# Kernel optimization log

Hardware: AMD Instinct MI355X
Metric: run time of the kernel (lower is better)

## Reference

```python
import jax, jax.numpy as jnp
import numpy as np

B, S, D = 8, 2048, 512
Q, K = 8, 1024


def setup_inputs() -> dict:
    key = jax.random.key(0)
    k1, k2 = jax.random.split(key)
    x = jax.random.normal(k1, (B, S, D), dtype=jnp.float32)
    codebooks = jax.random.normal(k2, (Q, K, D), dtype=jnp.float32) * 0.02
    return {"x": x, "codebooks": codebooks}


def reference(x, codebooks):
    """Residual VQ forward (eval mode): per level cdist + argmin + gather.

    Returns (quantized, indices, commitment_loss, perplexity) matching the
    torch module's output dict.
    """
    b, s, d = x.shape
    q_levels, k_codes, _ = codebooks.shape
    xf = x.reshape(-1, d)              # (N, D), N = b*s
    n_tok = xf.shape[0]

    def step(carry, codebook):
        residual, qsum = carry
        # squared euclidean distances: ||r||^2 - 2 r.C^T + ||c||^2  -> (N, K)
        dists = (
            jnp.sum(residual * residual, axis=-1, keepdims=True)
            - 2.0 * (residual @ codebook.T)
            + jnp.sum(codebook * codebook, axis=-1)[None, :]
        )
        idx = jnp.argmin(dists, axis=-1)          # (N,)
        quant = codebook[idx]                     # (N, D) gather
        commit = jnp.mean((residual - jax.lax.stop_gradient(quant)) ** 2)
        counts = jnp.zeros((k_codes,), x.dtype).at[idx].add(1.0)
        avg_probs = counts / n_tok
        perp = jnp.exp(-jnp.sum(avg_probs * jnp.log(avg_probs + 1e-10)))
        return (residual - quant, qsum + quant), (idx, commit, perp)

    (_, quantized_sum), (all_idx, commits, perps) = jax.lax.scan(
        step, (xf, jnp.zeros_like(xf)), codebooks
    )

    commitment_weight = 0.25
    commitment_loss = jnp.sum(commits) * commitment_weight
    perplexity = jnp.mean(perps)
    indices = jnp.transpose(all_idx).reshape(b, s, q_levels)  # (B, S, Q)
    # straight-through estimator
    quantized = x + jax.lax.stop_gradient(quantized_sum.reshape(b, s, d) - x)
    return quantized, indices, commitment_loss, perplexity
```

## Files before the change

### kernel.cpp

```cpp
#include <hip/hip_runtime.h>
#include <math.h>

#define NTOK 16384
#define DIM 512
#define QLV 8
#define KCODE 1024
#define BM 64
#define DC 8
#define NCH (DIM / DC)
#define TAU 1e-3f

#define NCK 16
#define CHUNKB 131072
#define CBSPLIT_FLOAT_OFF 65536
#define RCAP 16

typedef __attribute__((ext_vector_type(4))) float f32x4;
typedef __attribute__((ext_vector_type(8))) short bf16x8;

__global__ __launch_bounds__(256) void zero_ws(float* ws) {
  int i = blockIdx.x * 256 + threadIdx.x;
  for (int k = i; k < QLV * KCODE + 2 * QLV; k += gridDim.x * 256) ws[k] = 0.f;
}

__device__ __forceinline__ float np_blk128_sq(const float* __restrict__ x) {
#pragma clang fp contract(off)
  float L[16];
#pragma unroll
  for (int j = 0; j < 16; ++j) {
    const float a0 = x[j] * x[j];
    const float a1 = x[16 + j] * x[16 + j];
    const float a2 = x[32 + j] * x[32 + j];
    const float a3 = x[48 + j] * x[48 + j];
    const float a4 = x[64 + j] * x[64 + j];
    const float a5 = x[80 + j] * x[80 + j];
    const float a6 = x[96 + j] * x[96 + j];
    const float a7 = x[112 + j] * x[112 + j];
    L[j] = ((a0 + a1) + (a2 + a3)) + ((a4 + a5) + (a6 + a7));
  }
  float T3[8];
#pragma unroll
  for (int i = 0; i < 8; ++i) T3[i] = L[i] + L[i + 8];
  float T6[4];
#pragma unroll
  for (int j = 0; j < 4; ++j) T6[j] = T3[j] + T3[j + 4];
  return (T6[0] + T6[2]) + (T6[1] + T6[3]);
}

__device__ __forceinline__ float np_sum512_sq(const float* __restrict__ x) {
#pragma clang fp contract(off)
  const float p0 = np_blk128_sq(x);
  const float p1 = np_blk128_sq(x + 128);
  const float p2 = np_blk128_sq(x + 256);
  const float p3 = np_blk128_sq(x + 384);
  const float s01 = p0 + p1;
  const float s23 = p2 + p3;
  return s01 + s23;
}

__device__ __forceinline__ float np_dist(float A, const float* __restrict__ r,
                                         const float* __restrict__ c, float cn) {
#pragma clang fp contract(off)
  float b1 = 0.f;
#pragma unroll 8
  for (int d = 0; d < 384; ++d) b1 = __builtin_fmaf(r[d], c[d], b1);
  float b2 = 0.f;
#pragma unroll 8
  for (int d = 384; d < 512; ++d) b2 = __builtin_fmaf(r[d], c[d], b2);
  const float B = b1 + b2;
  const float t1 = 2.0f * B;
  const float t2 = A - t1;
  return t2 + cn;
}

__global__ __launch_bounds__(256) void cnorm_np_kernel(const float* __restrict__ cb,
                                                       float* __restrict__ cn) {
  const int row = blockIdx.x * 256 + threadIdx.x;
  cn[row] = np_sum512_sq(cb + (size_t)row * DIM);
}

__device__ __forceinline__ bool lt2(float a, int ia, float b, int ib) {
  return a < b || (a == b && ia < ib);
}

__device__ __forceinline__ unsigned short bf16_rtne(float x) {
  unsigned u = __builtin_bit_cast(unsigned, x);
  u += 0x7FFFu + ((u >> 16) & 1u);
  return (unsigned short)(u >> 16);
}
__device__ __forceinline__ float bf16_tof(unsigned short h) {
  unsigned u = (unsigned)h << 16;
  return __builtin_bit_cast(float, u);
}
__device__ __forceinline__ void split2(float x, unsigned short& h, unsigned short& l) {
  h = bf16_rtne(x);
  l = bf16_rtne(x - bf16_tof(h));
}

__device__ __forceinline__ void gload16(const void* g, void* l) {
  __builtin_amdgcn_global_load_lds(
      (const __attribute__((address_space(1))) unsigned int*)g,
      (__attribute__((address_space(3))) unsigned int*)l, 16, 0, 0);
}

__global__ __launch_bounds__(256) void split_cb_kernel(const float* __restrict__ cb,
                                                       unsigned short* __restrict__ dst) {
  const int f = blockIdx.x * 256 + threadIdx.x;
  const int d4 = f & 127;
  const int c = (f >> 7) & 1023;
  const int q = f >> 17;
  const float4 v = *(const float4*)(cb + (size_t)f * 4);
  const int d0 = d4 * 4;
  const int dc = d0 >> 5;
  const int e = d0 & 31;
  const int kb = e >> 3;
  const int e7 = e & 7;
  const int half = c >> 9, cl = c & 511;
  const int slot = kb ^ ((cl >> 1) & 3);
  const size_t base = (size_t)(q * NCK + dc) * CHUNKB + (size_t)half * 65536;
  const size_t off = base + (size_t)cl * 64 + (size_t)slot * 16 + (size_t)e7 * 2;
  unsigned short h0, l0, h1, l1, h2, l2, h3, l3;
  split2(v.x, h0, l0);
  split2(v.y, h1, l1);
  split2(v.z, h2, l2);
  split2(v.w, h3, l3);
  uint2 hv, lv;
  hv.x = (unsigned)h0 | ((unsigned)h1 << 16);
  hv.y = (unsigned)h2 | ((unsigned)h3 << 16);
  lv.x = (unsigned)l0 | ((unsigned)l1 << 16);
  lv.y = (unsigned)l2 | ((unsigned)l3 << 16);
  char* db = (char*)dst;
  *(uint2*)(db + off) = hv;
  *(uint2*)(db + off + 32768) = lv;
}

template <bool FIRST, bool LAST>
__global__ __launch_bounds__(512, 2) void level_mfma(
    const float* __restrict__ x, float* __restrict__ resid,
    const float* __restrict__ cb, const unsigned short* __restrict__ cbsplit,
    const float* __restrict__ cnorm, float* __restrict__ out_idx,
    float* __restrict__ counts, float* __restrict__ commit, int* __restrict__ rcnt,
    int* __restrict__ rlist, int* __restrict__ cand_cnt, int* __restrict__ cand,
    int have_cand, int qlev) {
  __shared__ __align__(16) unsigned char Bs[131072];
  __shared__ __align__(16) unsigned char As[16384];
  __shared__ __align__(16) float foldb[64][8][4];
  __shared__ int chosen[64];
  __shared__ float tieV1[64];
  __shared__ int ccnt[64];

  const int tid = threadIdx.x;
  const int lane = tid & 63;
  const int w = tid >> 6;
  const int col = lane & 15;
  const int kb = lane >> 4;
  const int blk = blockIdx.x;
  const float* rin = FIRST ? x : resid;
  const char* csp = (const char*)cbsplit;
  const size_t wl = (size_t)w * 8192 + (size_t)lane * 16;

  const int arow = tid >> 3;
  const int ae0 = (tid & 7) * 4;
  const int akb = ae0 >> 3;
  const int aslot = akb ^ ((arow >> 1) & 3);
  const size_t abyte = (size_t)arow * 64 + (size_t)aslot * 16 + (size_t)(ae0 & 7) * 2;
  const float* aglob = rin + (size_t)(blk * BM + arow) * DIM + ae0;

  f32x4 acc[2][4][4];
#pragma unroll
  for (int h = 0; h < 2; ++h)
#pragma unroll
    for (int j = 0; j < 4; ++j)
#pragma unroll
      for (int tf = 0; tf < 4; ++tf) acc[h][j][tf] = (f32x4){0.f, 0.f, 0.f, 0.f};

  {
    const float4 pA = *(const float4*)aglob;
    unsigned short h0, l0, h1, l1, h2, l2, h3, l3;
    split2(pA.x, h0, l0);
    split2(pA.y, h1, l1);
    split2(pA.z, h2, l2);
    split2(pA.w, h3, l3);
    uint2 hv, lv;
    hv.x = (unsigned)h0 | ((unsigned)h1 << 16);
    hv.y = (unsigned)h2 | ((unsigned)h3 << 16);
    lv.x = (unsigned)l0 | ((unsigned)l1 << 16);
    lv.y = (unsigned)l2 | ((unsigned)l3 << 16);
    *(uint2*)&As[abyte] = hv;
    *(uint2*)&As[4096 + abyte] = lv;
  }
  {
    const char* s = csp + wl;
    unsigned char* d = &Bs[(size_t)w * 8192];
#pragma unroll
    for (int i = 0; i < 8; ++i) gload16(s + i * 1024, d + i * 1024);
  }
  {
    const char* s = csp + 65536 + wl;
    unsigned char* d = &Bs[65536 + (size_t)w * 8192];
#pragma unroll
    for (int i = 0; i < 8; ++i) gload16(s + i * 1024, d + i * 1024);
  }
  asm volatile("s_waitcnt lgkmcnt(0)" ::: "memory");

  for (int dc = 0; dc < NCK; ++dc) {
    const int dn = (dc + 1) & (NCK - 1);
    const int abuf = dc & 1;
    const char* srcN = csp + (size_t)dn * CHUNKB;

    asm volatile("s_waitcnt vmcnt(8)" ::: "memory");
    asm volatile("s_barrier" ::: "memory");
    const float4 pAn = *(const float4*)(aglob + dn * 32);

    bf16x8 ah[4], al[4];
#pragma unroll
    for (int tf = 0; tf < 4; ++tf) {
      const int row = tf * 16 + col;
      const size_t slot16 = (size_t)((kb ^ ((row >> 1) & 3)) * 16);
      const size_t ab = (size_t)abuf * 8192 + (size_t)row * 64 + slot16;
      ah[tf] = *(const bf16x8*)&As[ab];
      al[tf] = *(const bf16x8*)&As[ab + 4096];
    }
    bf16x8 b0h[4], b0l[4];
#pragma unroll
    for (int j = 0; j < 4; ++j) {
      const int cl = (w + 8 * j) * 16 + col;
      const size_t bb = (size_t)cl * 64 + (size_t)((kb ^ ((cl >> 1) & 3)) * 16);
      b0h[j] = *(const bf16x8*)&Bs[bb];
      b0l[j] = *(const bf16x8*)&Bs[32768 + bb];
    }
    asm volatile("s_waitcnt lgkmcnt(0)" ::: "memory");
    __builtin_amdgcn_sched_barrier(0);
    __builtin_amdgcn_s_setprio(1);
#pragma unroll
    for (int j = 0; j < 4; ++j)
#pragma unroll
      for (int tf = 0; tf < 4; ++tf) {
        acc[0][j][tf] = __builtin_amdgcn_mfma_f32_16x16x32_bf16(ah[tf], b0h[j], acc[0][j][tf], 0, 0, 0);
        acc[0][j][tf] = __builtin_amdgcn_mfma_f32_16x16x32_bf16(al[tf], b0h[j], acc[0][j][tf], 0, 0, 0);
        acc[0][j][tf] = __builtin_amdgcn_mfma_f32_16x16x32_bf16(ah[tf], b0l[j], acc[0][j][tf], 0, 0, 0);
      }
    __builtin_amdgcn_s_setprio(0);
    asm volatile("s_barrier" ::: "memory");
    {
      const char* s = srcN + wl;
      unsigned char* d = &Bs[(size_t)w * 8192];
#pragma unroll
      for (int i = 0; i < 8; ++i) gload16(s + i * 1024, d + i * 1024);
    }

    asm volatile("s_waitcnt vmcnt(9)" ::: "memory");
    asm volatile("s_barrier" ::: "memory");
    {
      unsigned short h0, l0, h1, l1, h2, l2, h3, l3;
      split2(pAn.x, h0, l0);
      split2(pAn.y, h1, l1);
      split2(pAn.z, h2, l2);
      split2(pAn.w, h3, l3);
      uint2 hv, lv;
      hv.x = (unsigned)h0 | ((unsigned)h1 << 16);
      hv.y = (unsigned)h2 | ((unsigned)h3 << 16);
      lv.x = (unsigned)l0 | ((unsigned)l1 << 16);
      lv.y = (unsigned)l2 | ((unsigned)l3 << 16);
      const size_t ab0 = (size_t)(abuf ^ 1) * 8192 + abyte;
      *(uint2*)&As[ab0] = hv;
      *(uint2*)&As[ab0 + 4096] = lv;
    }
    bf16x8 b1h[4], b1l[4];
#pragma unroll
    for (int j = 0; j < 4; ++j) {
      const int cl = (w + 8 * j) * 16 + col;
      const size_t bb = (size_t)cl * 64 + (size_t)((kb ^ ((cl >> 1) & 3)) * 16);
      b1h[j] = *(const bf16x8*)&Bs[65536 + bb];
      b1l[j] = *(const bf16x8*)&Bs[65536 + 32768 + bb];
    }
    asm volatile("s_waitcnt lgkmcnt(0)" ::: "memory");
    __builtin_amdgcn_sched_barrier(0);
    __builtin_amdgcn_s_setprio(1);
#pragma unroll
    for (int j = 0; j < 4; ++j)
#pragma unroll
      for (int tf = 0; tf < 4; ++tf) {
        acc[1][j][tf] = __builtin_amdgcn_mfma_f32_16x16x32_bf16(ah[tf], b1h[j], acc[1][j][tf], 0, 0, 0);
        acc[1][j][tf] = __builtin_amdgcn_mfma_f32_16x16x32_bf16(al[tf], b1h[j], acc[1][j][tf], 0, 0, 0);
        acc[1][j][tf] = __builtin_amdgcn_mfma_f32_16x16x32_bf16(ah[tf], b1l[j], acc[1][j][tf], 0, 0, 0);
      }
    __builtin_amdgcn_s_setprio(0);
    asm volatile("s_barrier" ::: "memory");
    {
      const char* s = srcN + 65536 + wl;
      unsigned char* d = &Bs[65536 + (size_t)w * 8192];
#pragma unroll
      for (int i = 0; i < 8; ++i) gload16(s + i * 1024, d + i * 1024);
    }
  }
  __syncthreads();

  float cnv[2][4];
#pragma unroll
  for (int h = 0; h < 2; ++h)
#pragma unroll
    for (int j = 0; j < 4; ++j) cnv[h][j] = cnorm[(h * 32 + w + 8 * j) * 16 + col];

#pragma unroll
  for (int tf = 0; tf < 4; ++tf) {
#pragma unroll
    for (int r = 0; r < 4; ++r) {
      float b1 = 3.4e38f, b2 = 3.4e38f;
      int x1 = KCODE, x2 = KCODE;
#pragma unroll
      for (int h = 0; h < 2; ++h)
#pragma unroll
        for (int j = 0; j < 4; ++j) {
          const int c = (h * 32 + w + 8 * j) * 16 + col;
          const float dist = fmaf(-2.f, acc[h][j][tf][r], cnv[h][j]);
          if (lt2(dist, c, b1, x1)) {
            b2 = b1; x2 = x1; b1 = dist; x1 = c;
          } else if (lt2(dist, c, b2, x2)) {
            b2 = dist; x2 = c;
          }
        }
#pragma unroll
      for (int off = 1; off < 16; off <<= 1) {
        const float w1 = __shfl_xor(b1, off);
        const int j1 = __shfl_xor(x1, off);
        const float w2 = __shfl_xor(b2, off);
        const int j2 = __shfl_xor(x2, off);
        if (lt2(w1, j1, b1, x1)) {
          if (lt2(b1, x1, w2, j2)) { b2 = b1; x2 = x1; }
          else { b2 = w2; x2 = j2; }
          b1 = w1; x1 = j1;
        } else if (lt2(w1, j1, b2, x2)) {
          b2 = w1; x2 = j1;
        }
      }
      if (col == 0) {
        const int t = tf * 16 + (lane >> 4) * 4 + r;
        float4 fv;
        fv.x = b1; fv.y = __int_as_float(x1); fv.z = b2; fv.w = __int_as_float(x2);
        *(float4*)&foldb[t][w][0] = fv;
      }
    }
  }
  __syncthreads();

  if (tid < 64) {
    float V1 = 3.4e38f, V2 = 3.4e38f;
    int I1 = KCODE, I2 = KCODE;
#pragma unroll
    for (int ww = 0; ww < 8; ++ww) {
      const float4 e = *(const float4*)&foldb[tid][ww][0];
      const float a1 = e.x, a2 = e.z;
      const int a1i = __float_as_int(e.y), a2i = __float_as_int(e.w);
      if (lt2(a1, a1i, V1, I1)) {
        if (lt2(V1, I1, a2, a2i)) { V2 = V1; I2 = I1; }
        else { V2 = a2; I2 = a2i; }
        V1 = a1; I1 = a1i;
      } else if (lt2(a1, a1i, V2, I2)) {
        V2 = a1; I2 = a1i;
      }
    }
    ccnt[tid] = 0;
    tieV1[tid] = V1;
    if (V2 - V1 < TAU) {
      const int pos = atomicAdd(rcnt, 1);
      rlist[pos] = blk * BM + tid;
      chosen[tid] = -1;
    } else {
      chosen[tid] = I1;
      out_idx[(size_t)(blk * BM + tid) * QLV + qlev] = (float)I1;
      atomicAdd(&counts[I1], 1.0f);
    }
  }
  __syncthreads();

  if (have_cand) {
#pragma unroll
    for (int tf = 0; tf < 4; ++tf)
#pragma unroll
      for (int r = 0; r < 4; ++r) {
        const int t = tf * 16 + (lane >> 4) * 4 + r;
        if (chosen[t] != -1) continue;
        const float thr = tieV1[t] + TAU;
#pragma unroll
        for (int h = 0; h < 2; ++h)
#pragma unroll
          for (int j = 0; j < 4; ++j) {
            const float dist = fmaf(-2.f, acc[h][j][tf][r], cnv[h][j]);
            if (dist < thr) {
              const int c = (h * 32 + w + 8 * j) * 16 + col;
              const int pos = atomicAdd(&ccnt[t], 1);
              if (pos < RCAP) cand[(size_t)(blk * BM + t) * RCAP + pos] = c;
            }
          }
      }
    __syncthreads();
    if (tid < 64 && chosen[tid] == -1) cand_cnt[blk * BM + tid] = ccnt[tid];
  }

  {
    const int tb = tid >> 3, part = tid & 7;
    const size_t tok = (size_t)(blk * BM + tb);
    const int idx = chosen[tb];
    float sq = 0.f;
    if (idx >= 0) {
      const float4* cp = (const float4*)(cb + (size_t)idx * DIM);
      const float4* rp = (const float4*)(rin + tok * DIM);
      const float4* xp = (const float4*)(x + tok * DIM);
      float4* op = (float4*)(resid + tok * DIM);
#pragma unroll 4
      for (int kk = 0; kk < 16; ++kk) {
        const int d4 = part + kk * 8;
        const float4 r = rp[d4], c4 = cp[d4];
        float4 rn;
        rn.x = r.x - c4.x; rn.y = r.y - c4.y; rn.z = r.z - c4.z; rn.w = r.w - c4.w;
        sq += rn.x * rn.x + rn.y * rn.y + rn.z * rn.z + rn.w * rn.w;
        if (LAST) {
          const float4 xv = xp[d4];
          float4 qv;
          qv.x = xv.x - rn.x; qv.y = xv.y - rn.y; qv.z = xv.z - rn.z; qv.w = xv.w - rn.w;
          op[d4] = qv;
        } else {
          op[d4] = rn;
        }
      }
    }
#pragma unroll
    for (int off = 32; off; off >>= 1) sq += __shfl_down(sq, off);
    if (lane == 0) atomicAdd(commit, sq);
  }
}

template <bool FIRST, bool LAST>
__global__ __launch_bounds__(512, 2) void level_kernel(
    const float* __restrict__ x, float* __restrict__ resid,
    const float* __restrict__ cb, const float* __restrict__ cnorm,
    float* __restrict__ out_idx, float* __restrict__ counts,
    float* __restrict__ commit, int* __restrict__ rcnt,
    int* __restrict__ rlist, int qlev) {
  __shared__ float Rs[DC][BM + 4];
  __shared__ float Cs[DC][KCODE + 4];
  __shared__ int chosen[BM];

  const int tid = threadIdx.x;
  const int lane = tid & 63;
  const int ty = tid >> 6;
  const int tx = lane;
  const int blk = blockIdx.x;
  const float* rin = FIRST ? x : resid;

  float acc[8][16];
#pragma unroll
  for (int j = 0; j < 8; ++j)
#pragma unroll
    for (int g = 0; g < 16; ++g) acc[j][g] = 0.f;

  float4 pc[4];
  float4 pr;
  {
#pragma unroll
    for (int u = 0; u < 4; ++u) {
      const int f4 = tid + u * 512;
      const int code = f4 >> 1, d4 = f4 & 1;
      pc[u] = *(const float4*)(cb + (size_t)code * DIM + d4 * 4);
    }
    if (tid < 128) {
      const int tok = tid >> 1, d4 = tid & 1;
      pr = *(const float4*)(rin + (size_t)(blk * BM + tok) * DIM + d4 * 4);
    }
  }

  for (int dc = 0; dc < NCH; ++dc) {
    __syncthreads();
#pragma unroll
    for (int u = 0; u < 4; ++u) {
      const int f4 = tid + u * 512;
      const int code = f4 >> 1, d4 = f4 & 1;
      Cs[d4 * 4 + 0][code] = pc[u].x;
      Cs[d4 * 4 + 1][code] = pc[u].y;
      Cs[d4 * 4 + 2][code] = pc[u].z;
      Cs[d4 * 4 + 3][code] = pc[u].w;
    }
    if (tid < 128) {
      const int tok = tid >> 1, d4 = tid & 1;
      Rs[d4 * 4 + 0][tok] = pr.x;
      Rs[d4 * 4 + 1][tok] = pr.y;
      Rs[d4 * 4 + 2][tok] = pr.z;
      Rs[d4 * 4 + 3][tok] = pr.w;
    }
    if (dc + 1 < NCH) {
      const int doff = (dc + 1) * DC;
#pragma unroll
      for (int u = 0; u < 4; ++u) {
        const int f4 = tid + u * 512;
        const int code = f4 >> 1, d4 = f4 & 1;
        pc[u] = *(const float4*)(cb + (size_t)code * DIM + doff + d4 * 4);
      }
      if (tid < 128) {
        const int tok = tid >> 1, d4 = tid & 1;
        pr = *(const float4*)(rin + (size_t)(blk * BM + tok) * DIM + doff + d4 * 4);
      }
    }
    __syncthreads();
#pragma unroll
    for (int d = 0; d < DC; ++d) {
      const float4 ra = *(const float4*)&Rs[d][ty * 8];
      const float4 rb = *(const float4*)&Rs[d][ty * 8 + 4];
#pragma unroll
      for (int q = 0; q < 4; ++q) {
        const float4 cv = *(const float4*)&Cs[d][q * 256 + tx * 4];
        const float c0 = cv.x, c1 = cv.y, c2 = cv.z, c3 = cv.w;
        acc[0][q * 4 + 0] = fmaf(ra.x, c0, acc[0][q * 4 + 0]);
        acc[0][q * 4 + 1] = fmaf(ra.x, c1, acc[0][q * 4 + 1]);
        acc[0][q * 4 + 2] = fmaf(ra.x, c2, acc[0][q * 4 + 2]);
        acc[0][q * 4 + 3] = fmaf(ra.x, c3, acc[0][q * 4 + 3]);
        acc[1][q * 4 + 0] = fmaf(ra.y, c0, acc[1][q * 4 + 0]);
        acc[1][q * 4 + 1] = fmaf(ra.y, c1, acc[1][q * 4 + 1]);
        acc[1][q * 4 + 2] = fmaf(ra.y, c2, acc[1][q * 4 + 2]);
        acc[1][q * 4 + 3] = fmaf(ra.y, c3, acc[1][q * 4 + 3]);
        acc[2][q * 4 + 0] = fmaf(ra.z, c0, acc[2][q * 4 + 0]);
        acc[2][q * 4 + 1] = fmaf(ra.z, c1, acc[2][q * 4 + 1]);
        acc[2][q * 4 + 2] = fmaf(ra.z, c2, acc[2][q * 4 + 2]);
        acc[2][q * 4 + 3] = fmaf(ra.z, c3, acc[2][q * 4 + 3]);
        acc[3][q * 4 + 0] = fmaf(ra.w, c0, acc[3][q * 4 + 0]);
        acc[3][q * 4 + 1] = fmaf(ra.w, c1, acc[3][q * 4 + 1]);
        acc[3][q * 4 + 2] = fmaf(ra.w, c2, acc[3][q * 4 + 2]);
        acc[3][q * 4 + 3] = fmaf(ra.w, c3, acc[3][q * 4 + 3]);
        acc[4][q * 4 + 0] = fmaf(rb.x, c0, acc[4][q * 4 + 0]);
        acc[4][q * 4 + 1] = fmaf(rb.x, c1, acc[4][q * 4 + 1]);
        acc[4][q * 4 + 2] = fmaf(rb.x, c2, acc[4][q * 4 + 2]);
        acc[4][q * 4 + 3] = fmaf(rb.x, c3, acc[4][q * 4 + 3]);
        acc[5][q * 4 + 0] = fmaf(rb.y, c0, acc[5][q * 4 + 0]);
        acc[5][q * 4 + 1] = fmaf(rb.y, c1, acc[5][q * 4 + 1]);
        acc[5][q * 4 + 2] = fmaf(rb.y, c2, acc[5][q * 4 + 2]);
        acc[5][q * 4 + 3] = fmaf(rb.y, c3, acc[5][q * 4 + 3]);
        acc[6][q * 4 + 0] = fmaf(rb.z, c0, acc[6][q * 4 + 0]);
        acc[6][q * 4 + 1] = fmaf(rb.z, c1, acc[6][q * 4 + 1]);
        acc[6][q * 4 + 2] = fmaf(rb.z, c2, acc[6][q * 4 + 2]);
        acc[6][q * 4 + 3] = fmaf(rb.z, c3, acc[6][q * 4 + 3]);
        acc[7][q * 4 + 0] = fmaf(rb.w, c0, acc[7][q * 4 + 0]);
        acc[7][q * 4 + 1] = fmaf(rb.w, c1, acc[7][q * 4 + 1]);
        acc[7][q * 4 + 2] = fmaf(rb.w, c2, acc[7][q * 4 + 2]);
        acc[7][q * 4 + 3] = fmaf(rb.w, c3, acc[7][q * 4 + 3]);
      }
    }
  }

  float v1[8], v2[8];
  int i1[8], i2[8];
#pragma unroll
  for (int j = 0; j < 8; ++j) { v1[j] = v2[j] = 3.4e38f; i1[j] = i2[j] = KCODE; }
#pragma unroll
  for (int g = 0; g < 16; ++g) {
    const int c = (g >> 2) * 256 + tx * 4 + (g & 3);
    const float cn = cnorm[c];
#pragma unroll
    for (int j = 0; j < 8; ++j) {
      const float dist = fmaf(-2.f, acc[j][g], cn);
      if (lt2(dist, c, v1[j], i1[j])) {
        v2[j] = v1[j]; i2[j] = i1[j]; v1[j] = dist; i1[j] = c;
      } else if (lt2(dist, c, v2[j], i2[j])) {
        v2[j] = dist; i2[j] = c;
      }
    }
  }
#pragma unroll
  for (int off = 1; off < 64; off <<= 1) {
#pragma unroll
    for (int j = 0; j < 8; ++j) {
      const float w1 = __shfl_xor(v1[j], off);
      const int j1 = __shfl_xor(i1[j], off);
      const float w2 = __shfl_xor(v2[j], off);
      const int j2 = __shfl_xor(i2[j], off);
      if (lt2(w1, j1, v1[j], i1[j])) {
        if (lt2(v1[j], i1[j], w2, j2)) { v2[j] = v1[j]; i2[j] = i1[j]; }
        else { v2[j] = w2; i2[j] = j2; }
        v1[j] = w1; i1[j] = j1;
      } else {
        if (lt2(w1, j1, v2[j], i2[j])) { v2[j] = w1; i2[j] = j1; }
      }
    }
  }
  if (lane < 8) {
    const int tb = ty * 8 + lane;
    const float V1 = v1[lane], V2 = v2[lane];
    const int I1 = i1[lane];
    if (V2 - V1 < TAU) {
      const int pos = atomicAdd(rcnt, 1);
      rlist[pos] = blk * BM + tb;
      chosen[tb] = -1;
    } else {
      chosen[tb] = I1;
      out_idx[(size_t)(blk * BM + tb) * QLV + qlev] = (float)I1;
      atomicAdd(&counts[I1], 1.0f);
    }
  }
  __syncthreads();
  {
    const int tb = tid >> 3, part = tid & 7;
    const size_t tok = (size_t)(blk * BM + tb);
    const int idx = chosen[tb];
    float sq = 0.f;
    if (idx >= 0) {
      const float4* cp = (const float4*)(cb + (size_t)idx * DIM);
      const float4* rp = (const float4*)(rin + tok * DIM);
      const float4* xp = (const float4*)(x + tok * DIM);
      float4* op = (float4*)(resid + tok * DIM);
#pragma unroll 4
      for (int kk = 0; kk < 16; ++kk) {
        const int d4 = part + kk * 8;
        const float4 r = rp[d4], c4 = cp[d4];
        float4 rn;
        rn.x = r.x - c4.x; rn.y = r.y - c4.y; rn.z = r.z - c4.z; rn.w = r.w - c4.w;
        sq += rn.x * rn.x + rn.y * rn.y + rn.z * rn.z + rn.w * rn.w;
        if (LAST) {
          const float4 xv = xp[d4];
          float4 qv;
          qv.x = xv.x - rn.x; qv.y = xv.y - rn.y; qv.z = xv.z - rn.z; qv.w = xv.w - rn.w;
          op[d4] = qv;
        } else {
          op[d4] = rn;
        }
      }
    }
#pragma unroll
    for (int off = 32; off; off >>= 1) sq += __shfl_down(sq, off);
    if (lane == 0) atomicAdd(commit, sq);
  }
}

template <bool LAST>
__global__ __launch_bounds__(256) void rescue_np(
    const float* __restrict__ x, const float* __restrict__ rin,
    float* __restrict__ resid, const float* __restrict__ cbq,
    const float* __restrict__ cnq, float* __restrict__ out_idx,
    float* __restrict__ counts, float* __restrict__ commit,
    const int* __restrict__ rcnt, const int* __restrict__ rlist,
    const int* __restrict__ cand_cnt, const int* __restrict__ cand,
    int have_cand, int qlev) {
  __shared__ float rsh[DIM];
  __shared__ __align__(16) float crows[RCAP][DIM];
  __shared__ float sA;
  __shared__ float wv[4];
  __shared__ int wi[4];
  __shared__ int bestk_s;
  const int tid = threadIdx.x;
  const int n = rcnt[0];
  for (int it = blockIdx.x; it < n; it += gridDim.x) {
    const int t = rlist[it];
    rsh[tid] = rin[(size_t)t * DIM + tid];
    rsh[256 + tid] = rin[(size_t)t * DIM + 256 + tid];
    __syncthreads();
    if (tid == 0) sA = np_sum512_sq(rsh);
    __syncthreads();
    const float A = sA;
    float bv = 3.4e38f;
    int bi = KCODE;
    const int m = have_cand ? cand_cnt[t] : (RCAP + 1);
    if (m <= RCAP) {
      for (int c = 0; c < m; ++c) {
        const int k = cand[(size_t)t * RCAP + c];
        crows[c][tid] = cbq[(size_t)k * DIM + tid];
        crows[c][256 + tid] = cbq[(size_t)k * DIM + 256 + tid];
      }
      __syncthreads();
      for (int c = tid; c < m; c += 256) {
        const int k = cand[(size_t)t * RCAP + c];
        const float d = np_dist(A, rsh, &crows[c][0], cnq[k]);
        if (d < bv || (d == bv && k < bi)) { bv = d; bi = k; }
      }
    } else {
      for (int kk = 0; kk < 4; ++kk) {
        const int k = tid * 4 + kk;
        const float d = np_dist(A, rsh, cbq + (size_t)k * DIM, cnq[k]);
        if (d < bv) { bv = d; bi = k; }
      }
    }
#pragma unroll
    for (int off = 32; off; off >>= 1) {
      const float ov = __shfl_down(bv, off);
      const int oi = __shfl_down(bi, off);
      if (ov < bv || (ov == bv && oi < bi)) { bv = ov; bi = oi; }
    }
    if ((tid & 63) == 0) { wv[tid >> 6] = bv; wi[tid >> 6] = bi; }
    __syncthreads();
    if (tid == 0) {
      float V = wv[0]; int I = wi[0];
#pragma unroll
      for (int w = 1; w < 4; ++w)
        if (wv[w] < V || (wv[w] == V && wi[w] < I)) { V = wv[w]; I = wi[w]; }
      bestk_s = I;
      out_idx[(size_t)t * QLV + qlev] = (float)I;
      atomicAdd(&counts[I], 1.0f);
    }
    __syncthreads();
    const float* crow = cbq + (size_t)bestk_s * DIM;
    float sq;
    {
      const int d0 = tid, d1 = tid + 256;
      const float rn0 = rsh[d0] - crow[d0];
      const float rn1 = rsh[d1] - crow[d1];
      sq = rn0 * rn0 + rn1 * rn1;
      if (LAST) {
        resid[(size_t)t * DIM + d0] = x[(size_t)t * DIM + d0] - rn0;
        resid[(size_t)t * DIM + d1] = x[(size_t)t * DIM + d1] - rn1;
      } else {
        resid[(size_t)t * DIM + d0] = rn0;
        resid[(size_t)t * DIM + d1] = rn1;
      }
    }
#pragma unroll
    for (int off = 32; off; off >>= 1) sq += __shfl_down(sq, off);
    if ((tid & 63) == 0) wv[tid >> 6] = sq;
    __syncthreads();
    if (tid == 0)
      atomicAdd(commit, wv[0] + wv[1] + wv[2] + wv[3]);
    __syncthreads();
  }
}

__global__ __launch_bounds__(256) void finalize_scalars(const float* __restrict__ counts,
                                                        const float* __restrict__ commit,
                                                        float* __restrict__ out2) {
  const int tid = threadIdx.x;
  __shared__ float sh[4];
  __shared__ float perp_acc;
  if (tid == 0) perp_acc = 0.f;
  __syncthreads();
  for (int q = 0; q < QLV; ++q) {
    float h = 0.f;
    for (int k = tid; k < KCODE; k += 256) {
      const float p = counts[q * KCODE + k] * (1.0f / (float)NTOK);
      h += p * logf(p + 1e-10f);
    }
#pragma unroll
    for (int off = 32; off; off >>= 1) h += __shfl_down(h, off);
    if ((tid & 63) == 0) sh[tid >> 6] = h;
    __syncthreads();
    if (tid == 0) {
      const float H = sh[0] + sh[1] + sh[2] + sh[3];
      perp_acc += expf(-H);
    }
    __syncthreads();
  }
  if (tid == 0) {
    float closs = 0.f;
    for (int q = 0; q < QLV; ++q) closs += commit[q];
    out2[0] = closs * (0.25f / ((float)NTOK * (float)DIM));
    out2[1] = perp_acc * (1.0f / (float)QLV);
  }
}

extern "C" void kernel_launch(void* const* d_in, const int* in_sizes, int n_in,
                              void* d_out, int out_size, void* d_ws, size_t ws_size,
                              hipStream_t stream) {
  const float* x = (const float*)d_in[0];
  const float* cb = (const float*)d_in[1];
  float* out = (float*)d_out;
  float* ws = (float*)d_ws;

  float* resid = out;
  float* oidx = out + (size_t)NTOK * DIM;
  float* scal = oidx + (size_t)NTOK * QLV;
  float* counts = ws;
  float* commit = ws + QLV * KCODE;
  int* rcnt = (int*)(ws + QLV * KCODE + QLV);
  float* cnorm = ws + QLV * KCODE + 512;
  int* rlist = (int*)(ws + QLV * KCODE + 512 + QLV * KCODE);
  unsigned short* cbsplit = (unsigned short*)(ws + CBSPLIT_FLOAT_OFF);

  const size_t csplit_floats = (size_t)QLV * NCK * CHUNKB / 4;
  int* cand_cnt = (int*)(ws + CBSPLIT_FLOAT_OFF + csplit_floats);
  int* cand = cand_cnt + NTOK;
  const size_t need_mfma = ((size_t)CBSPLIT_FLOAT_OFF + csplit_floats) * 4;
  const size_t need_cand = need_mfma + (size_t)NTOK * (RCAP + 1) * 4;
  const bool use_mfma = ws_size >= need_mfma;
  const int have_cand = (use_mfma && ws_size >= need_cand) ? 1 : 0;

  hipLaunchKernelGGL(zero_ws, dim3(32), dim3(256), 0, stream, ws);
  hipLaunchKernelGGL(cnorm_np_kernel, dim3((QLV * KCODE) / 256), dim3(256), 0, stream,
                     cb, cnorm);
  if (use_mfma)
    hipLaunchKernelGGL(split_cb_kernel, dim3((QLV * KCODE * DIM / 4) / 256), dim3(256), 0,
                       stream, cb, cbsplit);

  for (int q = 0; q < QLV; ++q) {
    const float* cbq = cb + (size_t)q * KCODE * DIM;
    const float* cnq = cnorm + q * KCODE;
    float* ctq = counts + q * KCODE;
    float* cmq = commit + q;
    int* rcq = rcnt + q;
    const float* rin = (q == 0) ? x : resid;
    if (use_mfma) {
      const unsigned short* csq = cbsplit + (size_t)q * (NCK * CHUNKB / 2);
      if (q == 0)
        hipLaunchKernelGGL((level_mfma<true, false>), dim3(NTOK / BM), dim3(512), 0, stream,
                           x, resid, cbq, csq, cnq, oidx, ctq, cmq, rcq, rlist,
                           cand_cnt, cand, have_cand, q);
      else if (q == QLV - 1)
        hipLaunchKernelGGL((level_mfma<false, true>), dim3(NTOK / BM), dim3(512), 0, stream,
                           x, resid, cbq, csq, cnq, oidx, ctq, cmq, rcq, rlist,
                           cand_cnt, cand, have_cand, q);
      else
        hipLaunchKernelGGL((level_mfma<false, false>), dim3(NTOK / BM), dim3(512), 0, stream,
                           x, resid, cbq, csq, cnq, oidx, ctq, cmq, rcq, rlist,
                           cand_cnt, cand, have_cand, q);
    } else {
      if (q == 0)
        hipLaunchKernelGGL((level_kernel<true, false>), dim3(NTOK / BM), dim3(512), 0, stream,
                           x, resid, cbq, cnq, oidx, ctq, cmq, rcq, rlist, q);
      else if (q == QLV - 1)
        hipLaunchKernelGGL((level_kernel<false, true>), dim3(NTOK / BM), dim3(512), 0, stream,
                           x, resid, cbq, cnq, oidx, ctq, cmq, rcq, rlist, q);
      else
        hipLaunchKernelGGL((level_kernel<false, false>), dim3(NTOK / BM), dim3(512), 0, stream,
                           x, resid, cbq, cnq, oidx, ctq, cmq, rcq, rlist, q);
    }
    if (q == QLV - 1)
      hipLaunchKernelGGL((rescue_np<true>), dim3(256), dim3(256), 0, stream,
                         x, rin, resid, cbq, cnq, oidx, ctq, cmq, rcq, rlist,
                         cand_cnt, cand, have_cand, q);
    else
      hipLaunchKernelGGL((rescue_np<false>), dim3(256), dim3(256), 0, stream,
                         x, rin, resid, cbq, cnq, oidx, ctq, cmq, rcq, rlist,
                         cand_cnt, cand, have_cand, q);
  }
  hipLaunchKernelGGL(finalize_scalars, dim3(1), dim3(256), 0, stream, counts, commit, scal);
}
```

Measured before the change: 1.166 ms.

## Replace block-shared B double buffer with per-wave ring buffer streaming

```diff
diff --git a/kernel.cpp b/kernel.cpp
--- a/kernel.cpp
+++ b/kernel.cpp
@@ -134,6 +134,8 @@
   *(uint2*)(db + off + 32768) = lv;
 }
 
+#define VMW(N) asm volatile("s_waitcnt vmcnt(" #N ")" ::: "memory")
+
 template <bool FIRST, bool LAST>
 __global__ __launch_bounds__(512, 2) void level_mfma(
     const float* __restrict__ x, float* __restrict__ resid,
@@ -142,7 +144,7 @@
     float* __restrict__ counts, float* __restrict__ commit, int* __restrict__ rcnt,
     int* __restrict__ rlist, int* __restrict__ cand_cnt, int* __restrict__ cand,
     int have_cand, int qlev) {
-  __shared__ __align__(16) unsigned char Bs[131072];
+  __shared__ __align__(16) unsigned char Bring[8][8][2048];
   __shared__ __align__(16) unsigned char As[16384];
   __shared__ __align__(16) float foldb[64][8][4];
   __shared__ int chosen[64];
@@ -157,7 +159,21 @@
   const int blk = blockIdx.x;
   const float* rin = FIRST ? x : resid;
   const char* csp = (const char*)cbsplit;
-  const size_t wl = (size_t)w * 8192 + (size_t)lane * 16;
+  unsigned char* bringw = &Bring[w][0][0];
+  const int bcol = col * 64 + ((kb ^ ((col >> 1) & 3)) << 4);
+
+  size_t srcoff[8];
+#pragma unroll
+  for (int jp = 0; jp < 8; ++jp) {
+    const int cf = w + 8 * jp;
+    srcoff[jp] = (size_t)(cf >> 5) * 65536 + (size_t)(cf & 31) * 1024 + (size_t)lane * 16;
+  }
+  int rdA[4];
+#pragma unroll
+  for (int tf = 0; tf < 4; ++tf) {
+    const int row = tf * 16 + col;
+    rdA[tf] = row * 64 + ((kb ^ ((row >> 1) & 3)) << 4);
+  }
 
   const int arow = tid >> 3;
   const int ae0 = (tid & 7) * 4;
@@ -166,141 +182,107 @@
   const size_t abyte = (size_t)arow * 64 + (size_t)aslot * 16 + (size_t)(ae0 & 7) * 2;
   const float* aglob = rin + (size_t)(blk * BM + arow) * DIM + ae0;
 
-  f32x4 acc[2][4][4];
-#pragma unroll
-  for (int h = 0; h < 2; ++h)
-#pragma unroll
-    for (int j = 0; j < 4; ++j)
-#pragma unroll
-      for (int tf = 0; tf < 4; ++tf) acc[h][j][tf] = (f32x4){0.f, 0.f, 0.f, 0.f};
+  f32x4 acc[8][4];
+#pragma unroll
+  for (int j = 0; j < 8; ++j)
+#pragma unroll
+    for (int tf = 0; tf < 4; ++tf) acc[j][tf] = (f32x4){0.f, 0.f, 0.f, 0.f};
+
+#define LM_ISSUE(PDC, JP)                                          \
+  {                                                                \
+    const char* s_ = csp + (size_t)(PDC)*CHUNKB + srcoff[JP];      \
+    unsigned char* d_ = bringw + (JP)*2048;                        \
+    gload16(s_, d_);                                               \
+    gload16(s_ + 32768, d_ + 1024);                                \
+  }
+
+#define LM_COMPUTE(JJ)                                                                   \
+  {                                                                                      \
+    const unsigned char* sb_ = bringw + (JJ)*2048 + bcol;                                \
+    const bf16x8 bh_ = *(const bf16x8*)sb_;                                              \
+    const bf16x8 bl_ = *(const bf16x8*)(sb_ + 1024);                                     \
+    __builtin_amdgcn_s_setprio(1);                                                       \
+    _Pragma("unroll") for (int tf = 0; tf < 4; ++tf) {                                   \
+      acc[JJ][tf] = __builtin_amdgcn_mfma_f32_16x16x32_bf16(ah[tf], bh_, acc[JJ][tf], 0, 0, 0); \
+      acc[JJ][tf] = __builtin_amdgcn_mfma_f32_16x16x32_bf16(al[tf], bh_, acc[JJ][tf], 0, 0, 0); \
+      acc[JJ][tf] = __builtin_amdgcn_mfma_f32_16x16x32_bf16(ah[tf], bl_, acc[JJ][tf], 0, 0, 0); \
+    }                                                                                    \
+    __builtin_amdgcn_s_setprio(0);                                                       \
+  }
+
+#define LM_ASPLIT(BUF)                                             \
+  {                                                                \
+    unsigned short h0, l0, h1, l1, h2, l2, h3, l3;                 \
+    split2(pAn.x, h0, l0);                                         \
+    split2(pAn.y, h1, l1);                                         \
+    split2(pAn.z, h2, l2);                                         \
+    split2(pAn.w, h3, l3);                                         \
+    uint2 hv, lv;                                                  \
+    hv.x = (unsigned)h0 | ((unsigned)h1 << 16);                    \
+    hv.y = (unsigned)h2 | ((unsigned)h3 << 16);                    \
+    lv.x = (unsigned)l0 | ((unsigned)l1 << 16);                    \
+    lv.y = (unsigned)l2 | ((unsigned)l3 << 16);                    \
+    const size_t ab0_ = (size_t)(BUF)*8192 + abyte;                \
+    *(uint2*)&As[ab0_] = hv;                                       \
+    *(uint2*)&As[4096 + ab0_] = lv;                                \
+  }
 
   {
-    const float4 pA = *(const float4*)aglob;
-    unsigned short h0, l0, h1, l1, h2, l2, h3, l3;
-    split2(pA.x, h0, l0);
-    split2(pA.y, h1, l1);
-    split2(pA.z, h2, l2);
-    split2(pA.w, h3, l3);
-    uint2 hv, lv;
-    hv.x = (unsigned)h0 | ((unsigned)h1 << 16);
-    hv.y = (unsigned)h2 | ((unsigned)h3 << 16);
-    lv.x = (unsigned)l0 | ((unsigned)l1 << 16);
-    lv.y = (unsigned)l2 | ((unsigned)l3 << 16);
-    *(uint2*)&As[abyte] = hv;
-    *(uint2*)&As[4096 + abyte] = lv;
-  }
-  {
-    const char* s = csp + wl;
-    unsigned char* d = &Bs[(size_t)w * 8192];
-#pragma unroll
-    for (int i = 0; i < 8; ++i) gload16(s + i * 1024, d + i * 1024);
-  }
-  {
-    const char* s = csp + 65536 + wl;
-    unsigned char* d = &Bs[65536 + (size_t)w * 8192];
-#pragma unroll
-    for (int i = 0; i < 8; ++i) gload16(s + i * 1024, d + i * 1024);
+    const float4 pAn = *(const float4*)aglob;
+    LM_ISSUE(0, 0); LM_ISSUE(0, 1); LM_ISSUE(0, 2);
+    LM_ISSUE(0, 3); LM_ISSUE(0, 4); LM_ISSUE(0, 5);
+    LM_ASPLIT(0);
   }
   asm volatile("s_waitcnt lgkmcnt(0)" ::: "memory");
-
-  for (int dc = 0; dc < NCK; ++dc) {
-    const int dn = (dc + 1) & (NCK - 1);
+  __builtin_amdgcn_s_barrier();
+
+  for (int dc = 0; dc < NCK - 1; ++dc) {
     const int abuf = dc & 1;
-    const char* srcN = csp + (size_t)dn * CHUNKB;
-
-    asm volatile("s_waitcnt vmcnt(8)" ::: "memory");
-    asm volatile("s_barrier" ::: "memory");
-    const float4 pAn = *(const float4*)(aglob + dn * 32);
-
     bf16x8 ah[4], al[4];
 #pragma unroll
     for (int tf = 0; tf < 4; ++tf) {
-      const int row = tf * 16 + col;
-      const size_t slot16 = (size_t)((kb ^ ((row >> 1) & 3)) * 16);
-      const size_t ab = (size_t)abuf * 8192 + (size_t)row * 64 + slot16;
+      const size_t ab = (size_t)abuf * 8192 + (size_t)rdA[tf];
       ah[tf] = *(const bf16x8*)&As[ab];
       al[tf] = *(const bf16x8*)&As[ab + 4096];
     }
-    bf16x8 b0h[4], b0l[4];
-#pragma unroll
-    for (int j = 0; j < 4; ++j) {
-      const int cl = (w + 8 * j) * 16 + col;
-      const size_t bb = (size_t)cl * 64 + (size_t)((kb ^ ((cl >> 1) & 3)) * 16);
-      b0h[j] = *(const bf16x8*)&Bs[bb];
-      b0l[j] = *(const bf16x8*)&Bs[32768 + bb];
-    }
+    float4 pAn;
+    VMW(10); LM_ISSUE(dc, 6);
+    pAn = *(const float4*)(aglob + (dc + 1) * 32);
+    LM_COMPUTE(0);
+    VMW(11); LM_ISSUE(dc, 7);     LM_COMPUTE(1);
+    VMW(11); LM_ISSUE(dc + 1, 0); LM_COMPUTE(2);
+    VMW(11); LM_ISSUE(dc + 1, 1); LM_COMPUTE(3);
+    VMW(11); LM_ISSUE(dc + 1, 2); LM_COMPUTE(4);
+    VMW(11); LM_ISSUE(dc + 1, 3); LM_COMPUTE(5);
+    LM_ASPLIT(abuf ^ 1);
+    VMW(11); LM_ISSUE(dc + 1, 4); LM_COMPUTE(6);
+    VMW(10); LM_ISSUE(dc + 1, 5); LM_COMPUTE(7);
     asm volatile("s_waitcnt lgkmcnt(0)" ::: "memory");
-    __builtin_amdgcn_sched_barrier(0);
-    __builtin_amdgcn_s_setprio(1);
-#pragma unroll
-    for (int j = 0; j < 4; ++j)
-#pragma unroll
-      for (int tf = 0; tf < 4; ++tf) {
-        acc[0][j][tf] = __builtin_amdgcn_mfma_f32_16x16x32_bf16(ah[tf], b0h[j], acc[0][j][tf], 0, 0, 0);
-        acc[0][j][tf] = __builtin_amdgcn_mfma_f32_16x16x32_bf16(al[tf], b0h[j], acc[0][j][tf], 0, 0, 0);
-        acc[0][j][tf] = __builtin_amdgcn_mfma_f32_16x16x32_bf16(ah[tf], b0l[j], acc[0][j][tf], 0, 0, 0);
-      }
-    __builtin_amdgcn_s_setprio(0);
-    asm volatile("s_barrier" ::: "memory");
-    {
-      const char* s = srcN + wl;
-      unsigned char* d = &Bs[(size_t)w * 8192];
-#pragma unroll
-      for (int i = 0; i < 8; ++i) gload16(s + i * 1024, d + i * 1024);
-    }
-
-    asm volatile("s_waitcnt vmcnt(9)" ::: "memory");
-    asm volatile("s_barrier" ::: "memory");
-    {
-      unsigned short h0, l0, h1, l1, h2, l2, h3, l3;
-      split2(pAn.x, h0, l0);
-      split2(pAn.y, h1, l1);
-      split2(pAn.z, h2, l2);
-      split2(pAn.w, h3, l3);
-      uint2 hv, lv;
-      hv.x = (unsigned)h0 | ((unsigned)h1 << 16);
-      hv.y = (unsigned)h2 | ((unsigned)h3 << 16);
-      lv.x = (unsigned)l0 | ((unsigned)l1 << 16);
-      lv.y = (unsigned)l2 | ((unsigned)l3 << 16);
-      const size_t ab0 = (size_t)(abuf ^ 1) * 8192 + abyte;
-      *(uint2*)&As[ab0] = hv;
-      *(uint2*)&As[ab0 + 4096] = lv;
-    }
-    bf16x8 b1h[4], b1l[4];
-#pragma unroll
-    for (int j = 0; j < 4; ++j) {
-      const int cl = (w + 8 * j) * 16 + col;
-      const size_t bb = (size_t)cl * 64 + (size_t)((kb ^ ((cl >> 1) & 3)) * 16);
-      b1h[j] = *(const bf16x8*)&Bs[65536 + bb];
-      b1l[j] = *(const bf16x8*)&Bs[65536 + 32768 + bb];
-    }
-    asm volatile("s_waitcnt lgkmcnt(0)" ::: "memory");
-    __builtin_amdgcn_sched_barrier(0);
-    __builtin_amdgcn_s_setprio(1);
-#pragma unroll
-    for (int j = 0; j < 4; ++j)
-#pragma unroll
-      for (int tf = 0; tf < 4; ++tf) {
-        acc[1][j][tf] = __builtin_amdgcn_mfma_f32_16x16x32_bf16(ah[tf], b1h[j], acc[1][j][tf], 0, 0, 0);
-        acc[1][j][tf] = __builtin_amdgcn_mfma_f32_16x16x32_bf16(al[tf], b1h[j], acc[1][j][tf], 0, 0, 0);
-        acc[1][j][tf] = __builtin_amdgcn_mfma_f32_16x16x32_bf16(ah[tf], b1l[j], acc[1][j][tf], 0, 0, 0);
-      }
-    __builtin_amdgcn_s_setprio(0);
-    asm volatile("s_barrier" ::: "memory");
-    {
-      const char* s = srcN + 65536 + wl;
-      unsigned char* d = &Bs[65536 + (size_t)w * 8192];
-#pragma unroll
-      for (int i = 0; i < 8; ++i) gload16(s + i * 1024, d + i * 1024);
-    }
+    __builtin_amdgcn_s_barrier();
+  }
+
+  {
+    bf16x8 ah[4], al[4];
+#pragma unroll
+    for (int tf = 0; tf < 4; ++tf) {
+      const size_t ab = (size_t)8192 + (size_t)rdA[tf];
+      ah[tf] = *(const bf16x8*)&As[ab];
+      al[tf] = *(const bf16x8*)&As[ab + 4096];
+    }
+    VMW(10); LM_ISSUE(15, 6); LM_COMPUTE(0);
+    VMW(10); LM_ISSUE(15, 7); LM_COMPUTE(1);
+    VMW(10); LM_COMPUTE(2);
+    VMW(8);  LM_COMPUTE(3);
+    VMW(6);  LM_COMPUTE(4);
+    VMW(4);  LM_COMPUTE(5);
+    VMW(2);  LM_COMPUTE(6);
+    VMW(0);  LM_COMPUTE(7);
   }
   __syncthreads();
 
-  float cnv[2][4];
-#pragma unroll
-  for (int h = 0; h < 2; ++h)
-#pragma unroll
-    for (int j = 0; j < 4; ++j) cnv[h][j] = cnorm[(h * 32 + w + 8 * j) * 16 + col];
+  float cnv[8];
+#pragma unroll
+  for (int j = 0; j < 8; ++j) cnv[j] = cnorm[(w + 8 * j) * 16 + col];
 
 #pragma unroll
   for (int tf = 0; tf < 4; ++tf) {
@@ -309,17 +291,15 @@
       float b1 = 3.4e38f, b2 = 3.4e38f;
       int x1 = KCODE, x2 = KCODE;
 #pragma unroll
-      for (int h = 0; h < 2; ++h)
-#pragma unroll
-        for (int j = 0; j < 4; ++j) {
-          const int c = (h * 32 + w + 8 * j) * 16 + col;
-          const float dist = fmaf(-2.f, acc[h][j][tf][r], cnv[h][j]);
-          if (lt2(dist, c, b1, x1)) {
-            b2 = b1; x2 = x1; b1 = dist; x1 = c;
-          } else if (lt2(dist, c, b2, x2)) {
-            b2 = dist; x2 = c;
-          }
+      for (int j = 0; j < 8; ++j) {
+        const int c = (w + 8 * j) * 16 + col;
+        const float dist = fmaf(-2.f, acc[j][tf][r], cnv[j]);
+        if (lt2(dist, c, b1, x1)) {
+          b2 = b1; x2 = x1; b1 = dist; x1 = c;
+        } else if (lt2(dist, c, b2, x2)) {
+          b2 = dist; x2 = c;
         }
+      }
 #pragma unroll
       for (int off = 1; off < 16; off <<= 1) {
         const float w1 = __shfl_xor(b1, off);
@@ -383,16 +363,14 @@
         if (chosen[t] != -1) continue;
         const float thr = tieV1[t] + TAU;
 #pragma unroll
-        for (int h = 0; h < 2; ++h)
-#pragma unroll
-          for (int j = 0; j < 4; ++j) {
-            const float dist = fmaf(-2.f, acc[h][j][tf][r], cnv[h][j]);
-            if (dist < thr) {
-              const int c = (h * 32 + w + 8 * j) * 16 + col;
-              const int pos = atomicAdd(&ccnt[t], 1);
-              if (pos < RCAP) cand[(size_t)(blk * BM + t) * RCAP + pos] = c;
-            }
+        for (int j = 0; j < 8; ++j) {
+          const float dist = fmaf(-2.f, acc[j][tf][r], cnv[j]);
+          if (dist < thr) {
+            const int c = (w + 8 * j) * 16 + col;
+            const int pos = atomicAdd(&ccnt[t], 1);
+            if (pos < RCAP) cand[(size_t)(blk * BM + t) * RCAP + pos] = c;
           }
+        }
       }
     __syncthreads();
     if (tid < 64 && chosen[tid] == -1) cand_cnt[blk * BM + tid] = ccnt[tid];
@@ -430,6 +408,9 @@
     if (lane == 0) atomicAdd(commit, sq);
   }
 }
+#undef LM_ISSUE
+#undef LM_COMPUTE
+#undef LM_ASPLIT
 
 template <bool FIRST, bool LAST>
 __global__ __launch_bounds__(512, 2) void level_kernel(
```

Measured after the change: 1.057 ms. 9.3% less time.
